# Kernel tuning notes

Hardware: AMD Instinct MI355X
Metric: run time of the kernel (lower is better)

Reference implementation:

```python
import jax, jax.numpy as jnp
import numpy as np

B, DIN, N = 8, 256, 2048  # batch, input_dim (orig node_num), attention nodes (orig seq_len)


def setup_inputs() -> dict:
    key = jax.random.key(0)
    k1, k2, k3, k4 = jax.random.split(key, 4)
    x = jax.random.normal(k1, (B, DIN, N), jnp.float32)
    adj = jax.random.randint(k2, (N, N), 0, 2).astype(jnp.int32)  # binary adjacency
    W = jax.random.normal(k3, (DIN, DIN), jnp.float32) * 0.05      # Linear(D, D, bias=False), stored (out, in)
    a = jax.random.normal(k4, (3 * DIN,), jnp.float32) * 0.05      # Linear(3D, 1, bias=False)
    return {"x": x, "adj": adj, "W": W, "a": a}


def reference(x, adj, W, a):
    # x: (B, D, N) -> permute to (B, N, D); attention is over the N axis
    xt = jnp.transpose(x, (0, 2, 1))
    h = xt @ W.T                                   # (B, N, D)
    sim = jnp.einsum('bid,bjd->bij', h, h)         # (B, N, N) pairwise dot products
    n = adj.shape[0]
    # neighbor mask: adj nonzero, diagonal forced off (mask[:, i] = 0 in the loop)
    m = (adj != 0) & (~jnp.eye(n, dtype=bool))
    # context: the torch loop's weighted_h is independent of its k axis, so
    # context[b, k, i, d] == C[b, i, d] = sum_j m[i,j] * sim[b,i,j] * h[b,j,d]
    C = jnp.einsum('bij,bjd->bid', jnp.where(m[None, :, :], sim, 0.0), h)  # (B, N, D)
    d = h.shape[-1]
    a1, a2, a3 = a[:d], a[d:2 * d], a[2 * d:]
    # a([h_i, h_j, C_j]) = a1.h_i + a2.h_j + a3.C_j  (concat never materialized)
    s_i = h @ a1                                   # (B, N)
    s_j = h @ a2 + C @ a3                          # (B, N)
    scores = jax.nn.leaky_relu(s_i[:, :, None] + s_j[:, None, :], negative_slope=0.2)
    scores = jnp.where(adj[None, :, :] == 0, jnp.float32(-9e15), scores)
    return jax.nn.softmax(scores, axis=-1)         # (B, N, N)
```

## Files before the change

### kernel.cpp

```cpp
#include <hip/hip_runtime.h>
#include <hip/hip_bf16.h>
#include <math.h>

#define Bq   8
#define DINq 256
#define Nq   2048

typedef __attribute__((ext_vector_type(8))) short bf16x8v;
typedef __attribute__((ext_vector_type(4))) float f32x4v;

__device__ __forceinline__ unsigned short f2bf(float f) {
  union { float f; unsigned u; } v; v.f = f;
  unsigned r = v.u + 0x7fffu + ((v.u >> 16) & 1u);
  return (unsigned short)(r >> 16);
}
__device__ __forceinline__ float bf2f(unsigned short h) {
  union { unsigned u; float f; } v; v.u = ((unsigned)h) << 16;
  return v.f;
}

__device__ __forceinline__ void gld_lds16(const void* g, void* l) {
  __builtin_amdgcn_global_load_lds(
      (const __attribute__((address_space(1))) unsigned int*)g,
      (__attribute__((address_space(3))) unsigned int*)l, 16, 0, 0);
}

__global__ void k_prep(const float* __restrict__ W, const float* __restrict__ a,
                       float* __restrict__ w123) {
  int k = threadIdx.x;
  float s1 = 0.f, s2 = 0.f, s3 = 0.f;
  for (int d = 0; d < DINq; ++d) {
    float w = W[d * DINq + k];
    s1 += w * a[d];
    s2 += w * a[DINq + d];
    s3 += w * a[2 * DINq + d];
  }
  w123[k] = s1; w123[DINq + k] = s2; w123[2 * DINq + k] = s3;
}

__global__ void k_transposeW(const float* __restrict__ W, float* __restrict__ WT) {
  int d = blockIdx.x, k = threadIdx.x;
  WT[(size_t)k * DINq + d] = W[(size_t)d * DINq + k];
}

__global__ void k_hX(const float* __restrict__ x, const float* __restrict__ WT,
                     const float* __restrict__ w123, float* __restrict__ h,
                     unsigned short* __restrict__ Xhi, unsigned short* __restrict__ Xlo,
                     float* __restrict__ siA, float* __restrict__ sbA) {
  __shared__ float xs[64][64];
  __shared__ float ws[64][128];
  __shared__ float wls[3][256];
  __shared__ float Pd[3][16][64];
  __shared__ float Tt[64];
  const int tid = threadIdx.x;
  const int iq = tid & 15;
  const int dg = tid >> 4;
  const int i0 = blockIdx.x * 64;
  const int dh = blockIdx.y;
  const int b = blockIdx.z;

  for (int n = tid; n < 768; n += 256) ((float*)wls)[n] = w123[n];

  float acc[4][8];
#pragma unroll
  for (int aa = 0; aa < 4; ++aa)
#pragma unroll
    for (int cc = 0; cc < 8; ++cc) acc[aa][cc] = 0.f;
  float p1[4] = {0.f, 0.f, 0.f, 0.f}, p2[4] = {0.f, 0.f, 0.f, 0.f},
        p3[4] = {0.f, 0.f, 0.f, 0.f};

  for (int kc = 0; kc < 4; ++kc) {
#pragma unroll
    for (int n = 0; n < 16; ++n) {
      int idx = n * 256 + tid;
      int kk = idx >> 6, ii = idx & 63;
      xs[kk][ii] = x[((size_t)b * DINq + kc * 64 + kk) * Nq + i0 + ii];
    }
#pragma unroll
    for (int n = 0; n < 8; ++n) {
      int idx = n * 256 + tid;
      int kk = idx >> 5, c4 = (idx & 31) * 4;
      *(f32x4v*)&ws[kk][c4] =
          *(const f32x4v*)&WT[(size_t)(kc * 64 + kk) * DINq + dh * 128 + c4];
    }
    __syncthreads();
#pragma unroll 4
    for (int kk = 0; kk < 64; ++kk) {
      f32x4v xv = *(const f32x4v*)&xs[kk][iq * 4];
      f32x4v w0 = *(const f32x4v*)&ws[kk][dg * 8];
      f32x4v w1 = *(const f32x4v*)&ws[kk][dg * 8 + 4];
#pragma unroll
      for (int aa = 0; aa < 4; ++aa) {
#pragma unroll
        for (int cc = 0; cc < 4; ++cc) {
          acc[aa][cc]     += xv[aa] * w0[cc];
          acc[aa][cc + 4] += xv[aa] * w1[cc];
        }
      }
    }
#pragma unroll
    for (int kap = 0; kap < 4; ++kap) {
      int kk = dg * 4 + kap;
      f32x4v xv = *(const f32x4v*)&xs[kk][iq * 4];
      float w3 = wls[2][kc * 64 + kk];
#pragma unroll
      for (int aa = 0; aa < 4; ++aa) p3[aa] += xv[aa] * w3;
      if (dh == 0) {
        float w1 = wls[0][kc * 64 + kk], w2 = wls[1][kc * 64 + kk];
#pragma unroll
        for (int aa = 0; aa < 4; ++aa) { p1[aa] += xv[aa] * w1; p2[aa] += xv[aa] * w2; }
      }
    }
    __syncthreads();
  }

#pragma unroll
  for (int aa = 0; aa < 4; ++aa) {
    Pd[2][dg][iq * 4 + aa] = p3[aa];
    if (dh == 0) { Pd[0][dg][iq * 4 + aa] = p1[aa]; Pd[1][dg][iq * 4 + aa] = p2[aa]; }
  }
  __syncthreads();
  if (tid < 64) {
    float t = 0.f, s1 = 0.f, s2 = 0.f;
#pragma unroll
    for (int g = 0; g < 16; ++g) {
      t += Pd[2][g][tid];
      if (dh == 0) { s1 += Pd[0][g][tid]; s2 += Pd[1][g][tid]; }
    }
    Tt[tid] = t;
    if (dh == 0) {
      siA[(size_t)b * Nq + i0 + tid] = s1;
      sbA[(size_t)b * Nq + i0 + tid] = s2;
    }
  }
  __syncthreads();

  const int ib = i0 + iq * 4;
  float tv[4];
#pragma unroll
  for (int aa = 0; aa < 4; ++aa) tv[aa] = Tt[iq * 4 + aa];

#pragma unroll
  for (int aa = 0; aa < 4; ++aa) {
    size_t hoff = ((size_t)b * Nq + ib + aa) * DINq + dh * 128 + dg * 8;
    f32x4v h0, h1;
#pragma unroll
    for (int cc = 0; cc < 4; ++cc) { h0[cc] = acc[aa][cc]; h1[cc] = acc[aa][cc + 4]; }
    *(f32x4v*)&h[hoff] = h0;
    *(f32x4v*)&h[hoff + 4] = h1;
  }
#pragma unroll
  for (int cc = 0; cc < 8; ++cc) {
    int d = dh * 128 + dg * 8 + cc;
    unsigned short hv[4], lv[4];
#pragma unroll
    for (int aa = 0; aa < 4; ++aa) {
      float Xv = tv[aa] * acc[aa][cc];
      unsigned short hs = f2bf(Xv);
      hv[aa] = hs;
      lv[aa] = f2bf(Xv - bf2f(hs));
    }
    size_t xoff = ((size_t)b * DINq + d) * Nq + ib;
    *(ushort4*)&Xhi[xoff] = make_ushort4(hv[0], hv[1], hv[2], hv[3]);
    *(ushort4*)&Xlo[xoff] = make_ushort4(lv[0], lv[1], lv[2], lv[3]);
  }
}

__global__ void k_mask(const int* __restrict__ adj, unsigned short* __restrict__ Mb,
                       unsigned* __restrict__ bm) {
  int wg = blockIdx.x * 256 + threadIdx.x;
  int i = wg >> 6, w = wg & 63, j0 = w * 32;
  const int4* ap = (const int4*)&adj[(size_t)i * Nq + j0];
  unsigned bits = 0;
  unsigned short mv[32];
#pragma unroll
  for (int q = 0; q < 8; ++q) {
    int4 a = ap[q];
    int av[4] = {a.x, a.y, a.z, a.w};
#pragma unroll
    for (int e = 0; e < 4; ++e) {
      int j = j0 + q * 4 + e;
      bool nz = (av[e] != 0);
      if (nz) bits |= 1u << (q * 4 + e);
      mv[q * 4 + e] = (nz && j != i) ? (unsigned short)0x3F80 : (unsigned short)0;
    }
  }
  ushort4* mp = (ushort4*)&Mb[(size_t)i * Nq + j0];
#pragma unroll
  for (int q = 0; q < 8; ++q)
    mp[q] = make_ushort4(mv[q * 4], mv[q * 4 + 1], mv[q * 4 + 2], mv[q * 4 + 3]);
  bm[wg] = bits;
}

__global__ __launch_bounds__(256, 2) void k_gemm(const unsigned short* __restrict__ Mb,
                                                 const unsigned short* __restrict__ Xhi,
                                                 const unsigned short* __restrict__ Xlo,
                                                 const float* __restrict__ h,
                                                 float* __restrict__ sjp) {
  __shared__ __align__(16) unsigned short As[3][256 * 32];
  __shared__ __align__(16) unsigned short Bs[3][128 * 32];
  const int tid = threadIdx.x;
  const int lane = tid & 63;
  const int wave = tid >> 6;
  const int wm = wave >> 1, wc = wave & 1;
  const int wg = blockIdx.x;
  const int lin = (wg & 7) * 64 + (wg >> 3);
  const int mt = lin >> 6;
  const int rem = lin & 63;
  const int ks = rem >> 5;
  const int z = (rem >> 4) & 1;
  const int ct = rem & 15;
  const int i0 = mt * 256, c0 = ct * 128, kbase = ks * 1024;
  const unsigned short* __restrict__ Xp = z ? Xlo : Xhi;
  const int r15 = lane & 15, kg = lane >> 4;
  const int kb = (kg * 16) ^ ((r15 & 3) << 4);

  f32x4v acc[8][4];
#pragma unroll
  for (int m = 0; m < 8; ++m)
#pragma unroll
    for (int n = 0; n < 4; ++n) acc[m][n] = (f32x4v)0.f;

  auto STAGE = [&](int buf, int t) {
    const int k0 = kbase + t * 32;
#pragma unroll
    for (int l = 0; l < 4; ++l) {
      const int pc = l * 256 + tid;
      const int row = pc >> 2, q = pc & 3;
      const int kc = 8 * (q ^ (row & 3));
      gld_lds16(&Mb[(size_t)(i0 + row) * Nq + k0 + kc], &As[buf][pc * 8]);
    }
#pragma unroll
    for (int l = 0; l < 2; ++l) {
      const int pc = l * 256 + tid;
      const int row = pc >> 2, q = pc & 3;
      const int kc = 8 * (q ^ (row & 3));
      gld_lds16(&Xp[(size_t)(c0 + row) * Nq + k0 + kc], &Bs[buf][pc * 8]);
    }
  };

  constexpr int NT = 32;
  STAGE(0, 0);
  STAGE(1, 1);
  int cb = 0, sb2 = 2;
  for (int t = 0; t < NT; ++t) {
    if (t + 1 < NT) {
      asm volatile("s_waitcnt vmcnt(6)" ::: "memory");
    } else {
      asm volatile("s_waitcnt vmcnt(0)" ::: "memory");
    }
    __builtin_amdgcn_sched_barrier(0);
    __builtin_amdgcn_s_barrier();
    __builtin_amdgcn_sched_barrier(0);
    if (t + 2 < NT) STAGE(sb2, t + 2);

    const char* Ab = (const char*)&As[cb][0];
    const char* Bb = (const char*)&Bs[cb][0];
    bf16x8v af[8], bf[4];
#pragma unroll
    for (int m = 0; m < 8; ++m)
      af[m] = *(const bf16x8v*)(Ab + (wm * 128 + m * 16 + r15) * 64 + kb);
#pragma unroll
    for (int n = 0; n < 4; ++n)
      bf[n] = *(const bf16x8v*)(Bb + (wc * 64 + n * 16 + r15) * 64 + kb);
    __builtin_amdgcn_s_setprio(1);
#pragma unroll
    for (int m = 0; m < 8; ++m)
#pragma unroll
      for (int n = 0; n < 4; ++n)
        acc[m][n] = __builtin_amdgcn_mfma_f32_16x16x32_bf16(af[m], bf[n], acc[m][n], 0, 0, 0);
    __builtin_amdgcn_s_setprio(0);
    cb = (cb == 2) ? 0 : cb + 1;
    sb2 = (sb2 == 2) ? 0 : sb2 + 1;
  }

  const int b = c0 >> 8;
  const int d0 = (c0 & 255) + wc * 64;
  const int re = (lane >> 4) * 4, ce = lane & 15;
  float s[8][4];
#pragma unroll
  for (int m = 0; m < 8; ++m)
#pragma unroll
    for (int r = 0; r < 4; ++r) s[m][r] = 0.f;
#pragma unroll
  for (int m = 0; m < 8; ++m) {
#pragma unroll
    for (int n = 0; n < 4; ++n) {
#pragma unroll
      for (int r = 0; r < 4; ++r) {
        float hv = h[((size_t)b * Nq + i0 + wm * 128 + m * 16 + re + r) * DINq + d0 + n * 16 + ce];
        s[m][r] += acc[m][n][r] * hv;
      }
    }
  }
#pragma unroll
  for (int o = 1; o < 16; o <<= 1) {
#pragma unroll
    for (int m = 0; m < 8; ++m)
#pragma unroll
      for (int r = 0; r < 4; ++r) s[m][r] += __shfl_xor(s[m][r], o, 64);
  }
  if (ce == 0) {
    const int slice = ks * 8 + z * 4 + (ct & 1) * 2 + wc;
    float* sp = sjp + ((size_t)slice * Bq + b) * Nq;
#pragma unroll
    for (int m = 0; m < 8; ++m)
#pragma unroll
      for (int r = 0; r < 4; ++r)
        sp[i0 + wm * 128 + m * 16 + re + r] = s[m][r];
  }
}

__global__ void k_sjsum(const float* __restrict__ sbA, const float* __restrict__ sjp,
                        float* __restrict__ sjvA) {
  int idx = blockIdx.x * 256 + threadIdx.x;
  float s = sbA[idx];
#pragma unroll
  for (int sl = 0; sl < 16; ++sl) s += sjp[(size_t)sl * Bq * Nq + idx];
  sjvA[idx] = s;
}

__global__ void k_softmax(const unsigned* __restrict__ bm, const float* __restrict__ siA,
                          const float* __restrict__ sjvA, float* __restrict__ out) {
  const int b = blockIdx.y, i = blockIdx.x, tid = threadIdx.x;
  const float siv = siA[(size_t)b * Nq + i];
  const unsigned* brow = bm + (size_t)i * 64;
  const float* sjb = sjvA + (size_t)b * Nq;
  const int bit = tid & 31;
  float sc[8];
  float mx = -3.0e38f;
#pragma unroll
  for (int s = 0; s < 8; ++s) {
    int j = s * 256 + tid;
    float v = siv + sjb[j];
    v = v > 0.f ? v : 0.2f * v;
    unsigned wv = brow[j >> 5];
    v = ((wv >> bit) & 1u) ? v : -9.0e15f;
    sc[s] = v;
    mx = fmaxf(mx, v);
  }
#pragma unroll
  for (int o = 32; o >= 1; o >>= 1) mx = fmaxf(mx, __shfl_xor(mx, o, 64));
  __shared__ float redm[4], reds[4];
  const int wave = tid >> 6, lane = tid & 63;
  if (lane == 0) redm[wave] = mx;
  __syncthreads();
  mx = fmaxf(fmaxf(redm[0], redm[1]), fmaxf(redm[2], redm[3]));
  float sum = 0.f, ex[8];
#pragma unroll
  for (int s = 0; s < 8; ++s) { ex[s] = expf(sc[s] - mx); sum += ex[s]; }
#pragma unroll
  for (int o = 32; o >= 1; o >>= 1) sum += __shfl_xor(sum, o, 64);
  if (lane == 0) reds[wave] = sum;
  __syncthreads();
  sum = reds[0] + reds[1] + reds[2] + reds[3];
  float inv = 1.f / sum;
  float* orow = out + ((size_t)b * Nq + i) * Nq;
#pragma unroll
  for (int s = 0; s < 8; ++s) orow[s * 256 + tid] = ex[s] * inv;
}

extern "C" void kernel_launch(void* const* d_in, const int* in_sizes, int n_in,
                              void* d_out, int out_size, void* d_ws, size_t ws_size,
                              hipStream_t stream) {
  const float* x = (const float*)d_in[0];
  const int* adj = (const int*)d_in[1];
  const float* W = (const float*)d_in[2];
  const float* a = (const float*)d_in[3];
  float* out = (float*)d_out;

  char* ws = (char*)d_ws;
  size_t off = 0;
  auto alloc = [&](size_t bytes) -> void* {
    void* p = ws + off;
    off += (bytes + 255) & ~(size_t)255;
    return p;
  };
  float* w123 = (float*)alloc(3 * DINq * sizeof(float));
  float* WT = (float*)alloc((size_t)DINq * DINq * sizeof(float));
  float* siA = (float*)alloc((size_t)Bq * Nq * sizeof(float));
  float* sbA = (float*)alloc((size_t)Bq * Nq * sizeof(float));
  float* sjvA = (float*)alloc((size_t)Bq * Nq * sizeof(float));
  float* sjp = (float*)alloc((size_t)16 * Bq * Nq * sizeof(float));
  float* h = (float*)alloc((size_t)Bq * Nq * DINq * sizeof(float));
  unsigned short* Xhi = (unsigned short*)alloc((size_t)Nq * Nq * 2);
  unsigned short* Xlo = (unsigned short*)alloc((size_t)Nq * Nq * 2);
  unsigned short* Mb = (unsigned short*)alloc((size_t)Nq * Nq * 2);
  unsigned* bm = (unsigned*)alloc((size_t)Nq * 64 * sizeof(unsigned));

  k_prep<<<dim3(1), dim3(256), 0, stream>>>(W, a, w123);
  k_transposeW<<<dim3(DINq), dim3(DINq), 0, stream>>>(W, WT);
  k_hX<<<dim3(Nq / 64, 2, Bq), dim3(256), 0, stream>>>(x, WT, w123, h, Xhi, Xlo, siA, sbA);
  k_mask<<<dim3(Nq * 64 / 256), dim3(256), 0, stream>>>(adj, Mb, bm);
  k_gemm<<<dim3(512), dim3(256), 0, stream>>>(Mb, Xhi, Xlo, h, sjp);
  k_sjsum<<<dim3(Bq * Nq / 256), dim3(256), 0, stream>>>(sbA, sjp, sjvA);
  k_softmax<<<dim3(Nq, Bq), dim3(256), 0, stream>>>(bm, siA, sjvA, out);
}
```

Measured before the change: 151.0 us.

## Drop fp32 h buffer; reconstruct h from bf16 hi/lo X in GEMM epilogue

Removes the fp32 h intermediate (B*N*D floats) entirely. The GEMM epilogue now rebuilds t*h from the bf16 hi/lo X arrays it already uses, and the sjsum kernel divides by the stored t to recover C·a3. The k_hX kernel is restructured so each block covers both D halves for 32 nodes, so the t reduction happens once per block. This saves the 16MB h write and read, but adds a division by t that is numerically risky if t is near zero, plus some precision loss from the bf16 reconstruction.

```diff
diff --git a/kernel.cpp b/kernel.cpp
--- a/kernel.cpp
+++ b/kernel.cpp
@@ -43,126 +43,111 @@
   WT[(size_t)k * DINq + d] = W[(size_t)d * DINq + k];
 }
 
-__global__ void k_hX(const float* __restrict__ x, const float* __restrict__ WT,
-                     const float* __restrict__ w123, float* __restrict__ h,
+__global__ __launch_bounds__(256, 2) void k_hX(const float* __restrict__ x,
+                     const float* __restrict__ WT, const float* __restrict__ w123,
                      unsigned short* __restrict__ Xhi, unsigned short* __restrict__ Xlo,
-                     float* __restrict__ siA, float* __restrict__ sbA) {
-  __shared__ float xs[64][64];
+                     float* __restrict__ tA, float* __restrict__ siA,
+                     float* __restrict__ sbA) {
+  __shared__ float xs[64][32];
   __shared__ float ws[64][128];
   __shared__ float wls[3][256];
-  __shared__ float Pd[3][16][64];
-  __shared__ float Tt[64];
+  __shared__ float Pd[3][16][32];
+  __shared__ float Tt[32];
   const int tid = threadIdx.x;
   const int iq = tid & 15;
   const int dg = tid >> 4;
-  const int i0 = blockIdx.x * 64;
-  const int dh = blockIdx.y;
-  const int b = blockIdx.z;
+  const int i0 = blockIdx.x * 32;
+  const int b = blockIdx.y;
 
   for (int n = tid; n < 768; n += 256) ((float*)wls)[n] = w123[n];
 
-  float acc[4][8];
-#pragma unroll
-  for (int aa = 0; aa < 4; ++aa)
-#pragma unroll
-    for (int cc = 0; cc < 8; ++cc) acc[aa][cc] = 0.f;
-  float p1[4] = {0.f, 0.f, 0.f, 0.f}, p2[4] = {0.f, 0.f, 0.f, 0.f},
-        p3[4] = {0.f, 0.f, 0.f, 0.f};
-
-  for (int kc = 0; kc < 4; ++kc) {
-#pragma unroll
-    for (int n = 0; n < 16; ++n) {
-      int idx = n * 256 + tid;
-      int kk = idx >> 6, ii = idx & 63;
-      xs[kk][ii] = x[((size_t)b * DINq + kc * 64 + kk) * Nq + i0 + ii];
-    }
-#pragma unroll
-    for (int n = 0; n < 8; ++n) {
-      int idx = n * 256 + tid;
-      int kk = idx >> 5, c4 = (idx & 31) * 4;
-      *(f32x4v*)&ws[kk][c4] =
-          *(const f32x4v*)&WT[(size_t)(kc * 64 + kk) * DINq + dh * 128 + c4];
-    }
-    __syncthreads();
+  float p1[2] = {0.f, 0.f}, p2[2] = {0.f, 0.f}, p3[2] = {0.f, 0.f};
+
+#pragma unroll
+  for (int dh = 0; dh < 2; ++dh) {
+    float acc[2][8];
+#pragma unroll
+    for (int aa = 0; aa < 2; ++aa)
+#pragma unroll
+      for (int cc = 0; cc < 8; ++cc) acc[aa][cc] = 0.f;
+
+    for (int kc = 0; kc < 4; ++kc) {
+      __syncthreads();
+#pragma unroll
+      for (int n = 0; n < 8; ++n) {
+        int idx = n * 256 + tid;
+        int kk = idx >> 5, ii = idx & 31;
+        xs[kk][ii] = x[((size_t)b * DINq + kc * 64 + kk) * Nq + i0 + ii];
+      }
+#pragma unroll
+      for (int n = 0; n < 8; ++n) {
+        int idx = n * 256 + tid;
+        int kk = idx >> 5, c4 = (idx & 31) * 4;
+        *(f32x4v*)&ws[kk][c4] =
+            *(const f32x4v*)&WT[(size_t)(kc * 64 + kk) * DINq + dh * 128 + c4];
+      }
+      __syncthreads();
 #pragma unroll 4
-    for (int kk = 0; kk < 64; ++kk) {
-      f32x4v xv = *(const f32x4v*)&xs[kk][iq * 4];
-      f32x4v w0 = *(const f32x4v*)&ws[kk][dg * 8];
-      f32x4v w1 = *(const f32x4v*)&ws[kk][dg * 8 + 4];
-#pragma unroll
-      for (int aa = 0; aa < 4; ++aa) {
+      for (int kk = 0; kk < 64; ++kk) {
+        float xv0 = xs[kk][iq * 2], xv1 = xs[kk][iq * 2 + 1];
+        f32x4v w0 = *(const f32x4v*)&ws[kk][dg * 8];
+        f32x4v w1 = *(const f32x4v*)&ws[kk][dg * 8 + 4];
 #pragma unroll
         for (int cc = 0; cc < 4; ++cc) {
-          acc[aa][cc]     += xv[aa] * w0[cc];
-          acc[aa][cc + 4] += xv[aa] * w1[cc];
+          acc[0][cc]     += xv0 * w0[cc];
+          acc[0][cc + 4] += xv0 * w1[cc];
+          acc[1][cc]     += xv1 * w0[cc];
+          acc[1][cc + 4] += xv1 * w1[cc];
         }
       }
-    }
-#pragma unroll
-    for (int kap = 0; kap < 4; ++kap) {
-      int kk = dg * 4 + kap;
-      f32x4v xv = *(const f32x4v*)&xs[kk][iq * 4];
-      float w3 = wls[2][kc * 64 + kk];
-#pragma unroll
-      for (int aa = 0; aa < 4; ++aa) p3[aa] += xv[aa] * w3;
       if (dh == 0) {
-        float w1 = wls[0][kc * 64 + kk], w2 = wls[1][kc * 64 + kk];
-#pragma unroll
-        for (int aa = 0; aa < 4; ++aa) { p1[aa] += xv[aa] * w1; p2[aa] += xv[aa] * w2; }
-      }
-    }
-    __syncthreads();
-  }
-
-#pragma unroll
-  for (int aa = 0; aa < 4; ++aa) {
-    Pd[2][dg][iq * 4 + aa] = p3[aa];
-    if (dh == 0) { Pd[0][dg][iq * 4 + aa] = p1[aa]; Pd[1][dg][iq * 4 + aa] = p2[aa]; }
-  }
-  __syncthreads();
-  if (tid < 64) {
-    float t = 0.f, s1 = 0.f, s2 = 0.f;
-#pragma unroll
-    for (int g = 0; g < 16; ++g) {
-      t += Pd[2][g][tid];
-      if (dh == 0) { s1 += Pd[0][g][tid]; s2 += Pd[1][g][tid]; }
-    }
-    Tt[tid] = t;
+#pragma unroll
+        for (int kap = 0; kap < 4; ++kap) {
+          int kk = dg * 4 + kap;
+          float xv0 = xs[kk][iq * 2], xv1 = xs[kk][iq * 2 + 1];
+          float w3 = wls[2][kc * 64 + kk];
+          float w1v = wls[0][kc * 64 + kk], w2v = wls[1][kc * 64 + kk];
+          p3[0] += xv0 * w3;  p3[1] += xv1 * w3;
+          p1[0] += xv0 * w1v; p1[1] += xv1 * w1v;
+          p2[0] += xv0 * w2v; p2[1] += xv1 * w2v;
+        }
+      }
+    }
+
     if (dh == 0) {
-      siA[(size_t)b * Nq + i0 + tid] = s1;
-      sbA[(size_t)b * Nq + i0 + tid] = s2;
-    }
-  }
-  __syncthreads();
-
-  const int ib = i0 + iq * 4;
-  float tv[4];
-#pragma unroll
-  for (int aa = 0; aa < 4; ++aa) tv[aa] = Tt[iq * 4 + aa];
-
-#pragma unroll
-  for (int aa = 0; aa < 4; ++aa) {
-    size_t hoff = ((size_t)b * Nq + ib + aa) * DINq + dh * 128 + dg * 8;
-    f32x4v h0, h1;
-#pragma unroll
-    for (int cc = 0; cc < 4; ++cc) { h0[cc] = acc[aa][cc]; h1[cc] = acc[aa][cc + 4]; }
-    *(f32x4v*)&h[hoff] = h0;
-    *(f32x4v*)&h[hoff + 4] = h1;
-  }
-#pragma unroll
-  for (int cc = 0; cc < 8; ++cc) {
-    int d = dh * 128 + dg * 8 + cc;
-    unsigned short hv[4], lv[4];
-#pragma unroll
-    for (int aa = 0; aa < 4; ++aa) {
-      float Xv = tv[aa] * acc[aa][cc];
-      unsigned short hs = f2bf(Xv);
-      hv[aa] = hs;
-      lv[aa] = f2bf(Xv - bf2f(hs));
-    }
-    size_t xoff = ((size_t)b * DINq + d) * Nq + ib;
-    *(ushort4*)&Xhi[xoff] = make_ushort4(hv[0], hv[1], hv[2], hv[3]);
-    *(ushort4*)&Xlo[xoff] = make_ushort4(lv[0], lv[1], lv[2], lv[3]);
+#pragma unroll
+      for (int aa = 0; aa < 2; ++aa) {
+        Pd[0][dg][iq * 2 + aa] = p1[aa];
+        Pd[1][dg][iq * 2 + aa] = p2[aa];
+        Pd[2][dg][iq * 2 + aa] = p3[aa];
+      }
+      __syncthreads();
+      if (tid < 32) {
+        float t = 0.f, s1 = 0.f, s2 = 0.f;
+#pragma unroll
+        for (int g = 0; g < 16; ++g) {
+          s1 += Pd[0][g][tid]; s2 += Pd[1][g][tid]; t += Pd[2][g][tid];
+        }
+        Tt[tid] = t;
+        tA[(size_t)b * Nq + i0 + tid] = t;
+        siA[(size_t)b * Nq + i0 + tid] = s1;
+        sbA[(size_t)b * Nq + i0 + tid] = s2;
+      }
+      __syncthreads();
+    }
+
+    const float tv0 = Tt[iq * 2], tv1 = Tt[iq * 2 + 1];
+#pragma unroll
+    for (int cc = 0; cc < 8; ++cc) {
+      int d = dh * 128 + dg * 8 + cc;
+      float X0 = tv0 * acc[0][cc];
+      float X1 = tv1 * acc[1][cc];
+      unsigned short h0 = f2bf(X0), h1 = f2bf(X1);
+      unsigned short l0 = f2bf(X0 - bf2f(h0)), l1 = f2bf(X1 - bf2f(h1));
+      size_t xoff = ((size_t)b * DINq + d) * Nq + i0 + iq * 2;
+      *(ushort2*)&Xhi[xoff] = make_ushort2(h0, h1);
+      *(ushort2*)&Xlo[xoff] = make_ushort2(l0, l1);
+    }
   }
 }
 
@@ -195,7 +180,6 @@
 __global__ __launch_bounds__(256, 2) void k_gemm(const unsigned short* __restrict__ Mb,
                                                  const unsigned short* __restrict__ Xhi,
                                                  const unsigned short* __restrict__ Xlo,
-                                                 const float* __restrict__ h,
                                                  float* __restrict__ sjp) {
   __shared__ __align__(16) unsigned short As[3][256 * 32];
   __shared__ __align__(16) unsigned short Bs[3][128 * 32];
@@ -275,7 +259,6 @@
   }
 
   const int b = c0 >> 8;
-  const int d0 = (c0 & 255) + wc * 64;
   const int re = (lane >> 4) * 4, ce = lane & 15;
   float s[8][4];
 #pragma unroll
@@ -283,14 +266,17 @@
 #pragma unroll
     for (int r = 0; r < 4; ++r) s[m][r] = 0.f;
 #pragma unroll
-  for (int m = 0; m < 8; ++m) {
-#pragma unroll
-    for (int n = 0; n < 4; ++n) {
-#pragma unroll
-      for (int r = 0; r < 4; ++r) {
-        float hv = h[((size_t)b * Nq + i0 + wm * 128 + m * 16 + re + r) * DINq + d0 + n * 16 + ce];
-        s[m][r] += acc[m][n][r] * hv;
-      }
+  for (int n = 0; n < 4; ++n) {
+    const size_t xrow = (size_t)(c0 + wc * 64 + n * 16 + ce) * Nq;
+#pragma unroll
+    for (int m = 0; m < 8; ++m) {
+      const size_t ib = xrow + i0 + wm * 128 + m * 16 + re;
+      ushort4 xh = *(const ushort4*)&Xhi[ib];
+      ushort4 xl = *(const ushort4*)&Xlo[ib];
+      s[m][0] += acc[m][n][0] * (bf2f(xh.x) + bf2f(xl.x));
+      s[m][1] += acc[m][n][1] * (bf2f(xh.y) + bf2f(xl.y));
+      s[m][2] += acc[m][n][2] * (bf2f(xh.z) + bf2f(xl.z));
+      s[m][3] += acc[m][n][3] * (bf2f(xh.w) + bf2f(xl.w));
     }
   }
 #pragma unroll
@@ -311,13 +297,13 @@
   }
 }
 
-__global__ void k_sjsum(const float* __restrict__ sbA, const float* __restrict__ sjp,
-                        float* __restrict__ sjvA) {
+__global__ void k_sjsum(const float* __restrict__ sbA, const float* __restrict__ tA,
+                        const float* __restrict__ sjp, float* __restrict__ sjvA) {
   int idx = blockIdx.x * 256 + threadIdx.x;
-  float s = sbA[idx];
+  float s = 0.f;
 #pragma unroll
   for (int sl = 0; sl < 16; ++sl) s += sjp[(size_t)sl * Bq * Nq + idx];
-  sjvA[idx] = s;
+  sjvA[idx] = sbA[idx] + s / tA[idx];
 }
 
 __global__ void k_softmax(const unsigned* __restrict__ bm, const float* __restrict__ siA,
@@ -378,11 +364,11 @@
   };
   float* w123 = (float*)alloc(3 * DINq * sizeof(float));
   float* WT = (float*)alloc((size_t)DINq * DINq * sizeof(float));
+  float* tA = (float*)alloc((size_t)Bq * Nq * sizeof(float));
   float* siA = (float*)alloc((size_t)Bq * Nq * sizeof(float));
   float* sbA = (float*)alloc((size_t)Bq * Nq * sizeof(float));
   float* sjvA = (float*)alloc((size_t)Bq * Nq * sizeof(float));
   float* sjp = (float*)alloc((size_t)16 * Bq * Nq * sizeof(float));
-  float* h = (float*)alloc((size_t)Bq * Nq * DINq * sizeof(float));
   unsigned short* Xhi = (unsigned short*)alloc((size_t)Nq * Nq * 2);
   unsigned short* Xlo = (unsigned short*)alloc((size_t)Nq * Nq * 2);
   unsigned short* Mb = (unsigned short*)alloc((size_t)Nq * Nq * 2);
@@ -390,9 +376,9 @@
 
   k_prep<<<dim3(1), dim3(256), 0, stream>>>(W, a, w123);
   k_transposeW<<<dim3(DINq), dim3(DINq), 0, stream>>>(W, WT);
-  k_hX<<<dim3(Nq / 64, 2, Bq), dim3(256), 0, stream>>>(x, WT, w123, h, Xhi, Xlo, siA, sbA);
+  k_hX<<<dim3(Nq / 32, Bq), dim3(256), 0, stream>>>(x, WT, w123, Xhi, Xlo, tA, siA, sbA);
   k_mask<<<dim3(Nq * 64 / 256), dim3(256), 0, stream>>>(adj, Mb, bm);
-  k_gemm<<<dim3(512), dim3(256), 0, stream>>>(Mb, Xhi, Xlo, h, sjp);
-  k_sjsum<<<dim3(Bq * Nq / 256), dim3(256), 0, stream>>>(sbA, sjp, sjvA);
+  k_gemm<<<dim3(512), dim3(256), 0, stream>>>(Mb, Xhi, Xlo, sjp);
+  k_sjsum<<<dim3(Bq * Nq / 256), dim3(256), 0, stream>>>(sbA, tA, sjp, sjvA);
   k_softmax<<<dim3(Nq, Bq), dim3(256), 0, stream>>>(bm, siA, sjvA, out);
 }
```

Result: no change. 148.9 us (-1.4%).
